# Kernel tuning notes

Measured on AMD Instinct MI355X. Metric: run time of the kernel, lower is better.

## Reference

```python
import jax, jax.numpy as jnp
import numpy as np

N = 16      # num_nodes
D = 128     # embedding_dim
H = 8       # num_heads
F = 512     # feedforward_dim
L = 4       # num_layers
IN = 64     # per-node input dim (joint_pos 32 + joint_vel 32)
B = 16384   # batch


def _ln(x, g, b):
    m = x.mean(-1, keepdims=True)
    v = ((x - m) ** 2).mean(-1, keepdims=True)
    return (x - m) * jax.lax.rsqrt(v + 1e-5) * g + b


def setup_inputs() -> dict:
    key = jax.random.key(0)
    ks = jax.random.split(key, 24)
    s = 0.02
    inp = {
        'joint_pos': jax.random.normal(ks[0], (B, 32), jnp.float32),
        'joint_vel': jax.random.normal(ks[1], (B, 32), jnp.float32),
        'adjacency': jax.random.randint(ks[2], (N, N), 0, 2).astype(jnp.int32),
        # per-node embedder (distinct Linear per node, stacked)
        'embed_W': jax.random.normal(ks[3], (N, IN, D), jnp.float32) * s,
        'embed_b': jnp.zeros((N, D), jnp.float32),
        'pos_emb': jax.random.normal(ks[4], (N, D), jnp.float32) * s,
        # per-layer attention params, stacked over layer dim
        'Wq': jax.random.normal(ks[5], (L, D, D), jnp.float32) * s,
        'bq': jnp.zeros((L, D), jnp.float32),
        'Wk': jax.random.normal(ks[6], (L, D, D), jnp.float32) * s,
        'bk': jnp.zeros((L, D), jnp.float32),
        'Wv': jax.random.normal(ks[7], (L, D, D), jnp.float32) * s,
        'bv': jnp.zeros((L, D), jnp.float32),
        'Wo': jax.random.normal(ks[8], (L, D, D), jnp.float32) * s,
        'bo': jnp.zeros((L, D), jnp.float32),
        'ln1_g': jnp.ones((L, D), jnp.float32),
        'ln1_b': jnp.zeros((L, D), jnp.float32),
        'ln2_g': jnp.ones((L, D), jnp.float32),
        'ln2_b': jnp.zeros((L, D), jnp.float32),
        'W1': jax.random.normal(ks[9], (L, D, F), jnp.float32) * s,
        'b1': jnp.zeros((L, F), jnp.float32),
        'W2': jax.random.normal(ks[10], (L, F, D), jnp.float32) * s,
        'b2': jnp.zeros((L, D), jnp.float32),
    }
    return inp


def reference(joint_pos, joint_vel, adjacency, embed_W, embed_b, pos_emb,
              Wq, bq, Wk, bk, Wv, bv, Wo, bo,
              ln1_g, ln1_b, ln2_g, ln2_b, W1, b1, W2, b2):
    # adjacency with forced self-loops -> additive attention mask [N, N]
    adj = adjacency.astype(bool) | jnp.eye(N, dtype=bool)
    mask = jnp.where(adj, 0.0, -jnp.inf).astype(jnp.float32)

    # every node sees the full concatenated obs (list-variant obs_node_dict)
    feats = jnp.concatenate([joint_pos, joint_vel], axis=-1)        # [B, IN]
    # distinct per-node linear embedders, batched as one einsum
    x = jnp.einsum('bi,nio->bno', feats, embed_W) + embed_b + pos_emb  # [B, N, D]

    dh = D // H
    scale = 1.0 / (dh ** 0.5)
    for l in range(L):  # BoT-Hard: mask on every layer; pre-LN
        h = _ln(x, ln1_g[l], ln1_b[l])
        q = (h @ Wq[l] + bq[l]).reshape(-1, N, H, dh)
        k = (h @ Wk[l] + bk[l]).reshape(-1, N, H, dh)
        v = (h @ Wv[l] + bv[l]).reshape(-1, N, H, dh)
        s = jnp.einsum('bnhd,bmhd->bhnm', q, k) * scale + mask       # [B, H, N, N]
        a = jax.nn.softmax(s, axis=-1)
        o = jnp.einsum('bhnm,bmhd->bnhd', a, v).reshape(-1, N, D)
        x = x + o @ Wo[l] + bo[l]
        h2 = _ln(x, ln2_g[l], ln2_b[l])
        x = x + jax.nn.relu(h2 @ W1[l] + b1[l]) @ W2[l] + b2[l]
    return x
```

## Files before the change

### kernel.cpp

```cpp
#include <hip/hip_runtime.h>
#include <stdint.h>

typedef __bf16 bf16;
typedef bf16 bf16x8 __attribute__((ext_vector_type(8)));
typedef bf16 bf16x4 __attribute__((ext_vector_type(4)));
typedef float f32x4 __attribute__((ext_vector_type(4)));
typedef uint32_t u32;
typedef uint8_t u8;

#define B_TOT 16384
#define SWG 8
#define NWGS (B_TOT / SWG)

__device__ __forceinline__ f32x4 mfma32(bf16x8 a, bf16x8 b, f32x4 c) {
  return __builtin_amdgcn_mfma_f32_16x16x32_bf16(a, b, c, 0, 0, 0);
}
__device__ __forceinline__ bf16x8 zero8() {
  bf16x8 v;
#pragma unroll
  for (int j = 0; j < 8; j++) v[j] = (bf16)0.f;
  return v;
}

__device__ __forceinline__ void bar_lg() {
  __builtin_amdgcn_sched_barrier(0);
  asm volatile("s_waitcnt lgkmcnt(0)" ::: "memory");
  __builtin_amdgcn_s_barrier();
  __builtin_amdgcn_sched_barrier(0);
}
__device__ __forceinline__ void bar_v0() {
  __builtin_amdgcn_sched_barrier(0);
  asm volatile("s_waitcnt vmcnt(0) lgkmcnt(0)" ::: "memory");
  __builtin_amdgcn_s_barrier();
  __builtin_amdgcn_sched_barrier(0);
}
__device__ __forceinline__ void bar_v2() {
  __builtin_amdgcn_sched_barrier(0);
  asm volatile("s_waitcnt vmcnt(2) lgkmcnt(0)" ::: "memory");
  __builtin_amdgcn_s_barrier();
  __builtin_amdgcn_sched_barrier(0);
}

__device__ __forceinline__ void stage16(const u8* __restrict__ src, int rowstride, int colbase,
                                        u8* dst, int tid) {
  __builtin_amdgcn_sched_barrier(0);
#pragma unroll
  for (int rr = 0; rr < 2; ++rr) {
    u32 o = (u32)(rr * 512 + tid) * 16u;
    u32 row = o >> 7, cb = o & 0x7Fu;
    const u8* s = src + (size_t)row * (size_t)rowstride + (size_t)colbase
                      + (size_t)(cb ^ ((row & 7u) << 4));
    __builtin_amdgcn_global_load_lds((const __attribute__((address_space(1))) u32*)s,
                                     (__attribute__((address_space(3))) u32*)(dst + o),
                                     16, 0, 0);
  }
}

__device__ __forceinline__ void st_row(u8* base, int row, int col, bf16 v) {
  *(bf16*)(base + (u32)(row * 256) + (u32)((2 * col) ^ ((row & 15) << 4))) = v;
}

__device__ __forceinline__ void loadA_rm(const u8* R, int g, int c, bf16x8 a[2][4]) {
  const u32 sw = (u32)c << 4;
#pragma unroll
  for (int mt = 0; mt < 2; ++mt)
#pragma unroll
    for (int ks = 0; ks < 4; ++ks)
      a[mt][ks] = *(const bf16x8*)(R + (u32)((mt * 16 + c) * 256)
                                     + (((u32)(ks * 64 + g * 16)) ^ sw));
}

__device__ __forceinline__ void gemm_half(const u8* Wb, int khalf, const bf16x8 a[2][4],
                                          f32x4 acc[2][4], int nh, int g, int c) {
  const u32 sw = (u32)(c & 7) << 4;
#pragma unroll
  for (int ksl = 0; ksl < 2; ++ksl) {
    int ks = khalf * 2 + ksl;
#pragma unroll
    for (int nt = 0; nt < 4; ++nt) {
      bf16x8 b = *(const bf16x8*)(Wb + (u32)((nh * 64 + nt * 16 + c) * 128)
                                     + (((u32)(ksl * 64 + g * 16)) ^ sw));
      acc[0][nt] = mfma32(a[0][ks], b, acc[0][nt]);
      acc[1][nt] = mfma32(a[1][ks], b, acc[1][nt]);
    }
  }
}

template <bool RELU>
__device__ __forceinline__ void epi_rm(const f32x4 acc[2][4], const float* __restrict__ bias,
                                       u8* Rdst, int nh, int g, int c) {
#pragma unroll
  for (int nt = 0; nt < 4; ++nt) {
    int col = nh * 64 + nt * 16 + c;
    float bb = bias[col];
#pragma unroll
    for (int mt = 0; mt < 2; ++mt)
#pragma unroll
      for (int r = 0; r < 4; ++r) {
        float v = acc[mt][nt][r] + bb;
        if (RELU) v = fmaxf(v, 0.f);
        st_row(Rdst, mt * 16 + 4 * g + r, col, (bf16)v);
      }
  }
}

__device__ __forceinline__ void pack4(const f32x4 v, u32& w0, u32& w1) {
  union { bf16 h[2]; u32 u; } t0, t1;
  t0.h[0] = (bf16)v[0]; t0.h[1] = (bf16)v[1];
  t1.h[0] = (bf16)v[2]; t1.h[1] = (bf16)v[3];
  w0 = t0.u; w1 = t1.u;
}

__device__ __forceinline__ bf16x8 Rfrag(u32 w0, u32 w1, int g, int c) {
  int s0 = 32 * g + c;
  int s1 = 32 * g + 16 + c;
  u32 a0 = (u32)__shfl((int)w0, s0);
  u32 a1 = (u32)__shfl((int)w1, s0);
  u32 a2 = (u32)__shfl((int)w0, s1);
  u32 a3 = (u32)__shfl((int)w1, s1);
  union { u32 u[4]; bf16x8 v; } r;
  bool ok = (g < 2);
  r.u[0] = ok ? a0 : 0u; r.u[1] = ok ? a1 : 0u;
  r.u[2] = ok ? a2 : 0u; r.u[3] = ok ? a3 : 0u;
  return r.v;
}

__device__ __forceinline__ void ln_part(const f32x4 x[2][4], float sS[2][4], float sS2[2][4]) {
#pragma unroll
  for (int mt = 0; mt < 2; ++mt) {
    f32x4 a = {0.f, 0.f, 0.f, 0.f}, b = {0.f, 0.f, 0.f, 0.f};
#pragma unroll
    for (int nt = 0; nt < 4; ++nt) { a += x[mt][nt]; b += x[mt][nt] * x[mt][nt]; }
#pragma unroll
    for (int r = 0; r < 4; ++r) {
      float s = a[r], s2 = b[r];
#pragma unroll
      for (int off = 1; off < 16; off <<= 1) { s += __shfl_xor(s, off); s2 += __shfl_xor(s2, off); }
      sS[mt][r] = s; sS2[mt][r] = s2;
    }
  }
}

__global__ void __launch_bounds__(512, 2)
bot_main(const int* __restrict__ adj,
         const float* __restrict__ embB, const float* __restrict__ posE,
         const float* __restrict__ pbq, const float* __restrict__ pbk,
         const float* __restrict__ pbv, const float* __restrict__ pbo,
         const float* __restrict__ l1g, const float* __restrict__ l1b,
         const float* __restrict__ l2g, const float* __restrict__ l2b,
         const float* __restrict__ pb1, const float* __restrict__ pb2,
         const bf16* __restrict__ feats, const bf16* __restrict__ embWT,
         const bf16* __restrict__ wqT, const bf16* __restrict__ wkT,
         const bf16* __restrict__ wvT, const bf16* __restrict__ woT,
         const bf16* __restrict__ w1T, const bf16* __restrict__ w2T,
         float* __restrict__ out) {
  __shared__ u8 smem[163840];
  const int tid = threadIdx.x;
  const int w = tid >> 6, lane = tid & 63, g = lane >> 4, c = lane & 15;
  const int p = w >> 1, nh = w & 1;
  const int S0 = blockIdx.x * SWG;

  u8* pairb = smem + p * 24576;
  u8* RA = pairb;
  u8* Rq = pairb + 8192;
  u8* Rk = pairb + 16384;
  u8* WB0 = smem + 98304;
  u8* WB1 = smem + 114688;
  u8* WB2 = smem + 131072;
  u8* WB3 = smem + 147456;
  float* scr = (float*)Rk;

  float maskT[4];
#pragma unroll
  for (int r = 0; r < 4; ++r) {
    int m = 4 * g + r;
    maskT[r] = (adj[c * 16 + m] != 0 || c == m) ? 0.f : -1e9f;
  }

  {
    float* x0 = (float*)smem;
    f32x4 ea[16] = {};
    bf16x8 af[2];
#pragma unroll
    for (int ks = 0; ks < 2; ++ks)
      af[ks] = *(const bf16x8*)(feats + (size_t)(S0 + (c & 7)) * 64 + ks * 32 + g * 8);
#pragma unroll
    for (int nt = 0; nt < 16; ++nt) {
#pragma unroll
      for (int ks = 0; ks < 2; ++ks) {
        bf16x8 bw = *(const bf16x8*)(embWT + (size_t)(w * 256 + nt * 16 + c) * 64 + ks * 32 + g * 8);
        ea[nt] = mfma32(af[ks], bw, ea[nt]);
      }
    }
    if (g < 2) {
#pragma unroll
      for (int nt = 0; nt < 16; ++nt)
#pragma unroll
        for (int r = 0; r < 4; ++r)
          x0[(4 * g + r) * 2048 + w * 256 + nt * 16 + c] = ea[nt][r];
    }
  }
  __syncthreads();

  f32x4 x[2][4];
  {
    const float* x0 = (const float*)smem;
#pragma unroll
    for (int nt = 0; nt < 4; ++nt)
#pragma unroll
      for (int r = 0; r < 4; ++r) {
        int n = 4 * g + r, d = nh * 64 + nt * 16 + c;
        float eb = embB[n * 128 + d] + posE[n * 128 + d];
#pragma unroll
        for (int mt = 0; mt < 2; ++mt)
          x[mt][nt][r] = x0[(2 * p + mt) * 2048 + n * 128 + d] + eb;
      }
  }
  __syncthreads();

  bf16x8 Ah[2][4], Ah2[2][4], Au[2][4];

#pragma unroll 1
  for (int l = 0; l < 4; ++l) {
    const u8* Wq_l = (const u8*)(wqT + (size_t)l * 16384);
    const u8* Wk_l = (const u8*)(wkT + (size_t)l * 16384);
    const u8* Wv_l = (const u8*)(wvT + (size_t)l * 16384);
    const u8* Wo_l = (const u8*)(woT + (size_t)l * 16384);
    const u8* W1_l = (const u8*)(w1T + (size_t)l * 65536);
    const u8* W2_l = (const u8*)(w2T + (size_t)l * 65536);

    float sS[2][4], sS2[2][4], mean[2][4], rstd[2][4];

    ln_part(x, sS, sS2);
    if (c == 0) {
#pragma unroll
      for (int mt = 0; mt < 2; ++mt)
#pragma unroll
        for (int r = 0; r < 4; ++r) {
          int row = mt * 16 + 4 * g + r;
          scr[(row * 2 + nh) * 2 + 0] = sS[mt][r];
          scr[(row * 2 + nh) * 2 + 1] = sS2[mt][r];
        }
    }
    stage16(Wq_l, 256, 0, WB0, tid);
    bar_lg();

#pragma unroll
    for (int mt = 0; mt < 2; ++mt)
#pragma unroll
      for (int r = 0; r < 4; ++r) {
        int row = mt * 16 + 4 * g + r;
        float s = sS[mt][r] + scr[(row * 2 + (1 - nh)) * 2 + 0];
        float s2 = sS2[mt][r] + scr[(row * 2 + (1 - nh)) * 2 + 1];
        float mu = s * (1.f / 128.f);
        float va = s2 * (1.f / 128.f) - mu * mu;
        mean[mt][r] = mu; rstd[mt][r] = rsqrtf(va + 1e-5f);
      }
#pragma unroll
    for (int nt = 0; nt < 4; ++nt) {
      int col = nh * 64 + nt * 16 + c;
      float gg = l1g[l * 128 + col], bb = l1b[l * 128 + col];
#pragma unroll
      for (int mt = 0; mt < 2; ++mt)
#pragma unroll
        for (int r = 0; r < 4; ++r)
          st_row(RA, mt * 16 + 4 * g + r, col,
                 (bf16)((x[mt][nt][r] - mean[mt][r]) * rstd[mt][r] * gg + bb));
    }
    stage16(Wq_l, 256, 128, WB1, tid);
    bar_v2();

    f32x4 acc[2][4];
    loadA_rm(RA, g, c, Ah);
#pragma unroll
    for (int mt = 0; mt < 2; ++mt)
#pragma unroll
      for (int nt = 0; nt < 4; ++nt) acc[mt][nt] = (f32x4){0.f, 0.f, 0.f, 0.f};
    gemm_half(WB0, 0, Ah, acc, nh, g, c);
    stage16(Wk_l, 256, 0, WB2, tid);
    bar_v2();

    gemm_half(WB1, 1, Ah, acc, nh, g, c);
    epi_rm<false>(acc, pbq + l * 128, Rq, nh, g, c);
    stage16(Wk_l, 256, 128, WB3, tid);
    bar_v2();

#pragma unroll
    for (int mt = 0; mt < 2; ++mt)
#pragma unroll
      for (int nt = 0; nt < 4; ++nt) acc[mt][nt] = (f32x4){0.f, 0.f, 0.f, 0.f};
    gemm_half(WB2, 0, Ah, acc, nh, g, c);
    stage16(Wv_l, 256, 0, WB0, tid);
    bar_v2();

    gemm_half(WB3, 1, Ah, acc, nh, g, c);
    epi_rm<false>(acc, pbk + l * 128, Rk, nh, g, c);
    stage16(Wv_l, 256, 128, WB1, tid);
    bar_v2();

#pragma unroll
    for (int mt = 0; mt < 2; ++mt)
#pragma unroll
      for (int nt = 0; nt < 4; ++nt) acc[mt][nt] = (f32x4){0.f, 0.f, 0.f, 0.f};
    gemm_half(WB0, 0, Ah, acc, nh, g, c);
    bar_v0();

    bf16x8 Vf[2][4];
    gemm_half(WB1, 1, Ah, acc, nh, g, c);
#pragma unroll
    for (int nt = 0; nt < 4; ++nt) {
      float bb = pbv[l * 128 + nh * 64 + nt * 16 + c];
#pragma unroll
      for (int mt = 0; mt < 2; ++mt) {
        f32x4 v;
#pragma unroll
        for (int r = 0; r < 4; ++r) v[r] = acc[mt][nt][r] + bb;
        u32 w0, w1; pack4(v, w0, w1);
        Vf[mt][nt] = Rfrag(w0, w1, g, c);
      }
    }
    stage16(Wo_l, 256, 0, WB2, tid);
    bar_lg();

    {
      const f32x4 zz = {0.f, 0.f, 0.f, 0.f};
      const u32 swa = (u32)c << 4;
#pragma unroll
      for (int hh = 0; hh < 4; ++hh) {
        const int gh = nh * 4 + hh;
        bf16x8 qf[2], kf[2];
#pragma unroll
        for (int mt = 0; mt < 2; ++mt) {
          if (g < 2) {
            qf[mt] = *(const bf16x8*)(Rq + (u32)((mt * 16 + c) * 256)
                                         + (((u32)(gh * 32 + g * 16)) ^ swa));
            kf[mt] = *(const bf16x8*)(Rk + (u32)((mt * 16 + c) * 256)
                                         + (((u32)(gh * 32 + g * 16)) ^ swa));
          } else { qf[mt] = zero8(); kf[mt] = zero8(); }
        }
#pragma unroll
        for (int mt = 0; mt < 2; ++mt) {
          f32x4 st = mfma32(kf[mt], qf[mt], zz);
          float pr[4];
#pragma unroll
          for (int r = 0; r < 4; ++r) pr[r] = st[r] * 0.25f + maskT[r];
          float mx = fmaxf(fmaxf(pr[0], pr[1]), fmaxf(pr[2], pr[3]));
          mx = fmaxf(mx, __shfl_xor(mx, 16));
          mx = fmaxf(mx, __shfl_xor(mx, 32));
          float sm = 0.f;
#pragma unroll
          for (int r = 0; r < 4; ++r) { pr[r] = __expf(pr[r] - mx); sm += pr[r]; }
          sm += __shfl_xor(sm, 16);
          sm += __shfl_xor(sm, 32);
          float pinv = __fdividef(1.f, sm);
          f32x4 pv;
#pragma unroll
          for (int r = 0; r < 4; ++r) pv[r] = pr[r] * pinv;
          u32 w0, w1; pack4(pv, w0, w1);
          bf16x8 Pf = Rfrag(w0, w1, g, c);
          f32x4 oo = mfma32(Vf[mt][hh], Pf, zz);
          pack4(oo, w0, w1);
          bf16x8 Of = Rfrag(w0, w1, g, c);
          if (g < 2)
            *(bf16x8*)(Rq + (u32)((mt * 16 + c) * 256)
                          + (((u32)(gh * 32 + g * 16)) ^ swa)) = Of;
        }
      }
    }
    stage16(Wo_l, 256, 128, WB3, tid);
    bar_v2();

    loadA_rm(Rq, g, c, Ah);
    gemm_half(WB2, 0, Ah, x, nh, g, c);
    bar_v0();

    gemm_half(WB3, 1, Ah, x, nh, g, c);
#pragma unroll
    for (int nt = 0; nt < 4; ++nt) {
      float bb = pbo[l * 128 + nh * 64 + nt * 16 + c];
#pragma unroll
      for (int mt = 0; mt < 2; ++mt)
#pragma unroll
        for (int r = 0; r < 4; ++r) x[mt][nt][r] += bb;
    }
    ln_part(x, sS, sS2);
    if (c == 0) {
#pragma unroll
      for (int mt = 0; mt < 2; ++mt)
#pragma unroll
        for (int r = 0; r < 4; ++r) {
          int row = mt * 16 + 4 * g + r;
          scr[(row * 2 + nh) * 2 + 0] = sS[mt][r];
          scr[(row * 2 + nh) * 2 + 1] = sS2[mt][r];
        }
    }
    stage16(W1_l, 256, 0, WB0, tid);
    bar_lg();

#pragma unroll
    for (int mt = 0; mt < 2; ++mt)
#pragma unroll
      for (int r = 0; r < 4; ++r) {
        int row = mt * 16 + 4 * g + r;
        float s = sS[mt][r] + scr[(row * 2 + (1 - nh)) * 2 + 0];
        float s2 = sS2[mt][r] + scr[(row * 2 + (1 - nh)) * 2 + 1];
        float mu = s * (1.f / 128.f);
        float va = s2 * (1.f / 128.f) - mu * mu;
        mean[mt][r] = mu; rstd[mt][r] = rsqrtf(va + 1e-5f);
      }
#pragma unroll
    for (int nt = 0; nt < 4; ++nt) {
      int col = nh * 64 + nt * 16 + c;
      float gg = l2g[l * 128 + col], bb = l2b[l * 128 + col];
#pragma unroll
      for (int mt = 0; mt < 2; ++mt)
#pragma unroll
        for (int r = 0; r < 4; ++r)
          st_row(RA, mt * 16 + 4 * g + r, col,
                 (bf16)((x[mt][nt][r] - mean[mt][r]) * rstd[mt][r] * gg + bb));
    }
    stage16(W1_l, 256, 128, WB1, tid);
    bar_v2();

#pragma unroll 1
    for (int fc = 0; fc < 4; ++fc) {
      f32x4 uacc[2][4];
#pragma unroll
      for (int mt = 0; mt < 2; ++mt)
#pragma unroll
        for (int nt = 0; nt < 4; ++nt) uacc[mt][nt] = (f32x4){0.f, 0.f, 0.f, 0.f};
      if (fc == 0) loadA_rm(RA, g, c, Ah2);
      gemm_half(WB0, 0, Ah2, uacc, nh, g, c);
      stage16(W2_l, 1024, fc * 256, WB2, tid);
      bar_v2();
      gemm_half(WB1, 1, Ah2, uacc, nh, g, c);
      epi_rm<true>(uacc, pb1 + l * 512 + fc * 128, Rq, nh, g, c);
      stage16(W2_l, 1024, fc * 256 + 128, WB3, tid);
      bar_v2();
      loadA_rm(Rq, g, c, Au);
      gemm_half(WB2, 0, Au, x, nh, g, c);
      if (fc < 3) { stage16(W1_l + (fc + 1) * 32768, 256, 0, WB0, tid); bar_v2(); }
      else bar_v0();
      gemm_half(WB3, 1, Au, x, nh, g, c);
      if (fc < 3) { stage16(W1_l + (fc + 1) * 32768, 256, 128, WB1, tid); bar_v2(); }
      else {
#pragma unroll
        for (int nt = 0; nt < 4; ++nt) {
          float bb = pb2[l * 128 + nh * 64 + nt * 16 + c];
#pragma unroll
          for (int mt = 0; mt < 2; ++mt)
#pragma unroll
            for (int r = 0; r < 4; ++r) x[mt][nt][r] += bb;
        }
        bar_lg();
      }
    }
  }

#pragma unroll
  for (int nt = 0; nt < 4; ++nt) {
    int col = nh * 64 + nt * 16 + c;
#pragma unroll
    for (int mt = 0; mt < 2; ++mt)
      *(f32x4*)(pairb + mt * 8192 + col * 64 + g * 16) = x[mt][nt];
  }
  bar_lg();
  {
    const int smp = S0 + 2 * p + nh;
    const u8* src = pairb + nh * 8192;
#pragma unroll
    for (int it = 0; it < 8; ++it) {
      int n = it * 2 + (lane >> 5);
      int slot = lane & 31;
      f32x4 v;
#pragma unroll
      for (int e = 0; e < 4; ++e)
        v[e] = *(const float*)(src + (u32)((slot * 4 + e) * 64 + n * 4));
      *(f32x4*)(out + (size_t)smp * 2048 + n * 128 + slot * 4) = v;
    }
  }
}

__global__ void prep_feats_k(const float* __restrict__ pos, const float* __restrict__ vel,
                             bf16* __restrict__ feats) {
  int i = blockIdx.x * 256 + threadIdx.x;
  if (i >= B_TOT * 64) return;
  int b = i >> 6, k = i & 63;
  float v = (k < 32) ? pos[b * 32 + k] : vel[b * 32 + (k - 32)];
  feats[i] = (bf16)v;
}

__global__ void prep_tr_k(const float* __restrict__ src, bf16* __restrict__ dst,
                          int R, int C, int total) {
  int i = blockIdx.x * 256 + threadIdx.x;
  if (i >= total) return;
  int rc = R * C;
  int m = i / rc, rem = i % rc;
  int cc = rem / R, rr = rem % R;
  dst[i] = (bf16)src[(size_t)m * rc + rr * C + cc];
}

extern "C" void kernel_launch(void* const* d_in, const int* in_sizes, int n_in,
                              void* d_out, int out_size, void* d_ws, size_t ws_size,
                              hipStream_t stream) {
  const float* jp  = (const float*)d_in[0];
  const float* jv  = (const float*)d_in[1];
  const int*   adj = (const int*)d_in[2];
  const float* eW  = (const float*)d_in[3];
  const float* eB  = (const float*)d_in[4];
  const float* pE  = (const float*)d_in[5];
  const float* Wq  = (const float*)d_in[6];  const float* bq = (const float*)d_in[7];
  const float* Wk  = (const float*)d_in[8];  const float* bk = (const float*)d_in[9];
  const float* Wv  = (const float*)d_in[10]; const float* bv = (const float*)d_in[11];
  const float* Wo  = (const float*)d_in[12]; const float* bo = (const float*)d_in[13];
  const float* g1  = (const float*)d_in[14]; const float* be1 = (const float*)d_in[15];
  const float* g2  = (const float*)d_in[16]; const float* be2 = (const float*)d_in[17];
  const float* W1  = (const float*)d_in[18]; const float* b1 = (const float*)d_in[19];
  const float* W2  = (const float*)d_in[20]; const float* b2 = (const float*)d_in[21];

  bf16* ws    = (bf16*)d_ws;
  bf16* feats = ws;
  bf16* embWT = ws + 1048576;
  bf16* wqT   = embWT + 131072;
  bf16* wkT   = wqT + 65536;
  bf16* wvT   = wkT + 65536;
  bf16* woT   = wvT + 65536;
  bf16* w1T   = woT + 65536;
  bf16* w2T   = w1T + 262144;

  prep_feats_k<<<(B_TOT * 64 + 255) / 256, 256, 0, stream>>>(jp, jv, feats);
  prep_tr_k<<<512, 256, 0, stream>>>(eW, embWT, 64, 128, 131072);
  prep_tr_k<<<256, 256, 0, stream>>>(Wq, wqT, 128, 128, 65536);
  prep_tr_k<<<256, 256, 0, stream>>>(Wk, wkT, 128, 128, 65536);
  prep_tr_k<<<256, 256, 0, stream>>>(Wv, wvT, 128, 128, 65536);
  prep_tr_k<<<256, 256, 0, stream>>>(Wo, woT, 128, 128, 65536);
  prep_tr_k<<<1024, 256, 0, stream>>>(W1, w1T, 128, 512, 262144);
  prep_tr_k<<<1024, 256, 0, stream>>>(W2, w2T, 512, 128, 262144);

  bot_main<<<NWGS, 512, 0, stream>>>(adj, eB, pE, bq, bk, bv, bo,
                                     g1, be1, g2, be2, b1, b2,
                                     feats, embWT, wqT, wkT, wvT, woT, w1T, w2T,
                                     (float*)d_out);
}
```

Before: 1.047 ms.

## Halve workgroup to 4 samples and 256 threads, triple-buffer weight staging in LDS

Each workgroup now handles 4 batch samples with 256 threads instead of 8 samples with 512, cutting LDS per block from 160KB to 80KB so more blocks can be resident per CU. Weight staging drops from four LDS buffers to three, rotated through the FFN loop, and each thread issues four async loads per stage with matching vmcnt(4) waits. The embedding phase is split into two passes per wave. The aim is higher occupancy and better latency hiding, at the cost of each staged weight tile being reused by half as many samples, which doubles global and L2 weight traffic.

```diff
diff --git a/kernel.cpp b/kernel.cpp
--- a/kernel.cpp
+++ b/kernel.cpp
@@ -9,7 +9,7 @@
 typedef uint8_t u8;
 
 #define B_TOT 16384
-#define SWG 8
+#define SWG 4
 #define NWGS (B_TOT / SWG)
 
 __device__ __forceinline__ f32x4 mfma32(bf16x8 a, bf16x8 b, f32x4 c) {
@@ -34,9 +34,9 @@
   __builtin_amdgcn_s_barrier();
   __builtin_amdgcn_sched_barrier(0);
 }
-__device__ __forceinline__ void bar_v2() {
-  __builtin_amdgcn_sched_barrier(0);
-  asm volatile("s_waitcnt vmcnt(2) lgkmcnt(0)" ::: "memory");
+__device__ __forceinline__ void bar_v4() {
+  __builtin_amdgcn_sched_barrier(0);
+  asm volatile("s_waitcnt vmcnt(4) lgkmcnt(0)" ::: "memory");
   __builtin_amdgcn_s_barrier();
   __builtin_amdgcn_sched_barrier(0);
 }
@@ -45,8 +45,8 @@
                                         u8* dst, int tid) {
   __builtin_amdgcn_sched_barrier(0);
 #pragma unroll
-  for (int rr = 0; rr < 2; ++rr) {
-    u32 o = (u32)(rr * 512 + tid) * 16u;
+  for (int rr = 0; rr < 4; ++rr) {
+    u32 o = (u32)(rr * 256 + tid) * 16u;
     u32 row = o >> 7, cb = o & 0x7Fu;
     const u8* s = src + (size_t)row * (size_t)rowstride + (size_t)colbase
                       + (size_t)(cb ^ ((row & 7u) << 4));
@@ -141,7 +141,7 @@
   }
 }
 
-__global__ void __launch_bounds__(512, 2)
+__global__ void __launch_bounds__(256, 2)
 bot_main(const int* __restrict__ adj,
          const float* __restrict__ embB, const float* __restrict__ posE,
          const float* __restrict__ pbq, const float* __restrict__ pbk,
@@ -154,21 +154,19 @@
          const bf16* __restrict__ wvT, const bf16* __restrict__ woT,
          const bf16* __restrict__ w1T, const bf16* __restrict__ w2T,
          float* __restrict__ out) {
-  __shared__ u8 smem[163840];
+  __shared__ u8 smem[81920];
   const int tid = threadIdx.x;
   const int w = tid >> 6, lane = tid & 63, g = lane >> 4, c = lane & 15;
   const int p = w >> 1, nh = w & 1;
   const int S0 = blockIdx.x * SWG;
 
-  u8* pairb = smem + p * 24576;
-  u8* RA = pairb;
-  u8* Rq = pairb + 8192;
-  u8* Rk = pairb + 16384;
-  u8* WB0 = smem + 98304;
-  u8* WB1 = smem + 114688;
-  u8* WB2 = smem + 131072;
-  u8* WB3 = smem + 147456;
-  float* scr = (float*)Rk;
+  u8* pairb = smem + p * 16384;
+  u8* Th = pairb;
+  u8* Tq = pairb + 8192;
+  u8* WB0 = smem + 32768;
+  u8* WB1 = smem + 49152;
+  u8* WB2 = smem + 65536;
+  float* scr = (float*)Tq;
 
   float maskT[4];
 #pragma unroll
@@ -179,25 +177,29 @@
 
   {
     float* x0 = (float*)smem;
-    f32x4 ea[16] = {};
     bf16x8 af[2];
 #pragma unroll
     for (int ks = 0; ks < 2; ++ks)
-      af[ks] = *(const bf16x8*)(feats + (size_t)(S0 + (c & 7)) * 64 + ks * 32 + g * 8);
-#pragma unroll
-    for (int nt = 0; nt < 16; ++nt) {
-#pragma unroll
-      for (int ks = 0; ks < 2; ++ks) {
-        bf16x8 bw = *(const bf16x8*)(embWT + (size_t)(w * 256 + nt * 16 + c) * 64 + ks * 32 + g * 8);
-        ea[nt] = mfma32(af[ks], bw, ea[nt]);
-      }
-    }
-    if (g < 2) {
-#pragma unroll
-      for (int nt = 0; nt < 16; ++nt)
-#pragma unroll
-        for (int r = 0; r < 4; ++r)
-          x0[(4 * g + r) * 2048 + w * 256 + nt * 16 + c] = ea[nt][r];
+      af[ks] = *(const bf16x8*)(feats + (size_t)(S0 + (c & 3)) * 64 + ks * 32 + g * 8);
+#pragma unroll
+    for (int pp = 0; pp < 2; ++pp) {
+      f32x4 ea[16] = {};
+#pragma unroll
+      for (int nt = 0; nt < 16; ++nt) {
+#pragma unroll
+        for (int ks = 0; ks < 2; ++ks) {
+          bf16x8 bw = *(const bf16x8*)(embWT
+              + (size_t)(w * 512 + pp * 256 + nt * 16 + c) * 64 + ks * 32 + g * 8);
+          ea[nt] = mfma32(af[ks], bw, ea[nt]);
+        }
+      }
+      if (g == 0) {
+#pragma unroll
+        for (int nt = 0; nt < 16; ++nt)
+#pragma unroll
+          for (int r = 0; r < 4; ++r)
+            x0[r * 2048 + w * 512 + pp * 256 + nt * 16 + c] = ea[nt][r];
+      }
     }
   }
   __syncthreads();
@@ -243,7 +245,7 @@
         }
     }
     stage16(Wq_l, 256, 0, WB0, tid);
-    bar_lg();
+    bar_v4();
 
 #pragma unroll
     for (int mt = 0; mt < 2; ++mt)
@@ -264,49 +266,49 @@
       for (int mt = 0; mt < 2; ++mt)
 #pragma unroll
         for (int r = 0; r < 4; ++r)
-          st_row(RA, mt * 16 + 4 * g + r, col,
+          st_row(Th, mt * 16 + 4 * g + r, col,
                  (bf16)((x[mt][nt][r] - mean[mt][r]) * rstd[mt][r] * gg + bb));
     }
     stage16(Wq_l, 256, 128, WB1, tid);
-    bar_v2();
+    bar_v4();
 
     f32x4 acc[2][4];
-    loadA_rm(RA, g, c, Ah);
+    loadA_rm(Th, g, c, Ah);
 #pragma unroll
     for (int mt = 0; mt < 2; ++mt)
 #pragma unroll
       for (int nt = 0; nt < 4; ++nt) acc[mt][nt] = (f32x4){0.f, 0.f, 0.f, 0.f};
     gemm_half(WB0, 0, Ah, acc, nh, g, c);
     stage16(Wk_l, 256, 0, WB2, tid);
-    bar_v2();
+    bar_v4();
 
     gemm_half(WB1, 1, Ah, acc, nh, g, c);
-    epi_rm<false>(acc, pbq + l * 128, Rq, nh, g, c);
-    stage16(Wk_l, 256, 128, WB3, tid);
-    bar_v2();
+    epi_rm<false>(acc, pbq + l * 128, Tq, nh, g, c);
+    stage16(Wk_l, 256, 128, WB0, tid);
+    bar_v4();
 
 #pragma unroll
     for (int mt = 0; mt < 2; ++mt)
 #pragma unroll
       for (int nt = 0; nt < 4; ++nt) acc[mt][nt] = (f32x4){0.f, 0.f, 0.f, 0.f};
     gemm_half(WB2, 0, Ah, acc, nh, g, c);
-    stage16(Wv_l, 256, 0, WB0, tid);
-    bar_v2();
-
-    gemm_half(WB3, 1, Ah, acc, nh, g, c);
-    epi_rm<false>(acc, pbk + l * 128, Rk, nh, g, c);
-    stage16(Wv_l, 256, 128, WB1, tid);
-    bar_v2();
+    stage16(Wv_l, 256, 0, WB1, tid);
+    bar_v4();
+
+    gemm_half(WB0, 1, Ah, acc, nh, g, c);
+    epi_rm<false>(acc, pbk + l * 128, Th, nh, g, c);
+    stage16(Wv_l, 256, 128, WB2, tid);
+    bar_v4();
 
 #pragma unroll
     for (int mt = 0; mt < 2; ++mt)
 #pragma unroll
       for (int nt = 0; nt < 4; ++nt) acc[mt][nt] = (f32x4){0.f, 0.f, 0.f, 0.f};
-    gemm_half(WB0, 0, Ah, acc, nh, g, c);
+    gemm_half(WB1, 0, Ah, acc, nh, g, c);
     bar_v0();
 
     bf16x8 Vf[2][4];
-    gemm_half(WB1, 1, Ah, acc, nh, g, c);
+    gemm_half(WB2, 1, Ah, acc, nh, g, c);
 #pragma unroll
     for (int nt = 0; nt < 4; ++nt) {
       float bb = pbv[l * 128 + nh * 64 + nt * 16 + c];
@@ -319,8 +321,8 @@
         Vf[mt][nt] = Rfrag(w0, w1, g, c);
       }
     }
-    stage16(Wo_l, 256, 0, WB2, tid);
-    bar_lg();
+    stage16(Wo_l, 256, 0, WB0, tid);
+    bar_v4();
 
     {
       const f32x4 zz = {0.f, 0.f, 0.f, 0.f};
@@ -332,9 +334,9 @@
 #pragma unroll
         for (int mt = 0; mt < 2; ++mt) {
           if (g < 2) {
-            qf[mt] = *(const bf16x8*)(Rq + (u32)((mt * 16 + c) * 256)
+            qf[mt] = *(const bf16x8*)(Tq + (u32)((mt * 16 + c) * 256)
                                          + (((u32)(gh * 32 + g * 16)) ^ swa));
-            kf[mt] = *(const bf16x8*)(Rk + (u32)((mt * 16 + c) * 256)
+            kf[mt] = *(const bf16x8*)(Th + (u32)((mt * 16 + c) * 256)
                                          + (((u32)(gh * 32 + g * 16)) ^ swa));
           } else { qf[mt] = zero8(); kf[mt] = zero8(); }
         }
@@ -362,19 +364,19 @@
           pack4(oo, w0, w1);
           bf16x8 Of = Rfrag(w0, w1, g, c);
           if (g < 2)
-            *(bf16x8*)(Rq + (u32)((mt * 16 + c) * 256)
+            *(bf16x8*)(Tq + (u32)((mt * 16 + c) * 256)
                           + (((u32)(gh * 32 + g * 16)) ^ swa)) = Of;
         }
       }
     }
-    stage16(Wo_l, 256, 128, WB3, tid);
-    bar_v2();
-
-    loadA_rm(Rq, g, c, Ah);
-    gemm_half(WB2, 0, Ah, x, nh, g, c);
+    stage16(Wo_l, 256, 128, WB1, tid);
+    bar_v4();
+
+    loadA_rm(Tq, g, c, Ah);
+    gemm_half(WB0, 0, Ah, x, nh, g, c);
     bar_v0();
 
-    gemm_half(WB3, 1, Ah, x, nh, g, c);
+    gemm_half(WB1, 1, Ah, x, nh, g, c);
 #pragma unroll
     for (int nt = 0; nt < 4; ++nt) {
       float bb = pbo[l * 128 + nh * 64 + nt * 16 + c];
@@ -394,8 +396,8 @@
           scr[(row * 2 + nh) * 2 + 1] = sS2[mt][r];
         }
     }
-    stage16(W1_l, 256, 0, WB0, tid);
-    bar_lg();
+    stage16(W1_l, 256, 0, WB2, tid);
+    bar_v4();
 
 #pragma unroll
     for (int mt = 0; mt < 2; ++mt)
@@ -416,12 +418,13 @@
       for (int mt = 0; mt < 2; ++mt)
 #pragma unroll
         for (int r = 0; r < 4; ++r)
-          st_row(RA, mt * 16 + 4 * g + r, col,
+          st_row(Th, mt * 16 + 4 * g + r, col,
                  (bf16)((x[mt][nt][r] - mean[mt][r]) * rstd[mt][r] * gg + bb));
     }
-    stage16(W1_l, 256, 128, WB1, tid);
-    bar_v2();
-
+    stage16(W1_l, 256, 128, WB0, tid);
+    bar_v4();
+
+    u8 *bA = WB2, *bB = WB0, *bC = WB1;
 #pragma unroll 1
     for (int fc = 0; fc < 4; ++fc) {
       f32x4 uacc[2][4];
@@ -429,20 +432,20 @@
       for (int mt = 0; mt < 2; ++mt)
 #pragma unroll
         for (int nt = 0; nt < 4; ++nt) uacc[mt][nt] = (f32x4){0.f, 0.f, 0.f, 0.f};
-      if (fc == 0) loadA_rm(RA, g, c, Ah2);
-      gemm_half(WB0, 0, Ah2, uacc, nh, g, c);
-      stage16(W2_l, 1024, fc * 256, WB2, tid);
-      bar_v2();
-      gemm_half(WB1, 1, Ah2, uacc, nh, g, c);
-      epi_rm<true>(uacc, pb1 + l * 512 + fc * 128, Rq, nh, g, c);
-      stage16(W2_l, 1024, fc * 256 + 128, WB3, tid);
-      bar_v2();
-      loadA_rm(Rq, g, c, Au);
-      gemm_half(WB2, 0, Au, x, nh, g, c);
-      if (fc < 3) { stage16(W1_l + (fc + 1) * 32768, 256, 0, WB0, tid); bar_v2(); }
+      if (fc == 0) loadA_rm(Th, g, c, Ah2);
+      gemm_half(bA, 0, Ah2, uacc, nh, g, c);
+      stage16(W2_l, 1024, fc * 256, bC, tid);
+      bar_v4();
+      gemm_half(bB, 1, Ah2, uacc, nh, g, c);
+      epi_rm<true>(uacc, pb1 + l * 512 + fc * 128, Tq, nh, g, c);
+      stage16(W2_l, 1024, fc * 256 + 128, bA, tid);
+      bar_v4();
+      loadA_rm(Tq, g, c, Au);
+      gemm_half(bC, 0, Au, x, nh, g, c);
+      if (fc < 3) { stage16(W1_l + (fc + 1) * 32768, 256, 0, bB, tid); bar_v4(); }
       else bar_v0();
-      gemm_half(WB3, 1, Au, x, nh, g, c);
-      if (fc < 3) { stage16(W1_l + (fc + 1) * 32768, 256, 128, WB1, tid); bar_v2(); }
+      gemm_half(bA, 1, Au, x, nh, g, c);
+      if (fc < 3) { stage16(W1_l + (fc + 1) * 32768, 256, 128, bC, tid); bar_v4(); }
       else {
 #pragma unroll
         for (int nt = 0; nt < 4; ++nt) {
@@ -454,6 +457,7 @@
         }
         bar_lg();
       }
+      u8* t = bA; bA = bB; bB = bC; bC = t;
     }
   }
 
@@ -537,7 +541,7 @@
   prep_tr_k<<<1024, 256, 0, stream>>>(W1, w1T, 128, 512, 262144);
   prep_tr_k<<<1024, 256, 0, stream>>>(W2, w2T, 512, 128, 262144);
 
-  bot_main<<<NWGS, 512, 0, stream>>>(adj, eB, pE, bq, bk, bv, bo,
+  bot_main<<<NWGS, 256, 0, stream>>>(adj, eB, pE, bq, bk, bv, bo,
                                      g1, be1, g2, be2, b1, b2,
                                      feats, embWT, wqT, wkT, wvT, woT, w1T, w2T,
                                      (float*)d_out);
```

Result: slower. 1.213 ms (+15.9%).

## Keep Q/K in registers, shrink LDS, and deepen weight prefetch pipeline

Applied to the files above, without the earlier changes.

Q and K projections are now computed transposed (weights as the A operand), and the results are packed straight into MFMA fragments via shuffles instead of being written to and re-read from LDS. This removes the Rk buffer and cuts shared memory from 160KB to 128KB. Weight staging is re-sequenced so Wo, W1 and W2 chunks are prefetched further ahead, with vmcnt(4) waits keeping two stages in flight. The final output stores use nontemporal hints. Register pressure rises from holding Qb and Ka fragments, and the deeper prefetch depends on the vmcnt accounting being exactly right.

```diff
diff --git a/kernel.cpp b/kernel.cpp
--- a/kernel.cpp
+++ b/kernel.cpp
@@ -15,12 +15,6 @@
 __device__ __forceinline__ f32x4 mfma32(bf16x8 a, bf16x8 b, f32x4 c) {
   return __builtin_amdgcn_mfma_f32_16x16x32_bf16(a, b, c, 0, 0, 0);
 }
-__device__ __forceinline__ bf16x8 zero8() {
-  bf16x8 v;
-#pragma unroll
-  for (int j = 0; j < 8; j++) v[j] = (bf16)0.f;
-  return v;
-}
 
 __device__ __forceinline__ void bar_lg() {
   __builtin_amdgcn_sched_barrier(0);
@@ -37,6 +31,12 @@
 __device__ __forceinline__ void bar_v2() {
   __builtin_amdgcn_sched_barrier(0);
   asm volatile("s_waitcnt vmcnt(2) lgkmcnt(0)" ::: "memory");
+  __builtin_amdgcn_s_barrier();
+  __builtin_amdgcn_sched_barrier(0);
+}
+__device__ __forceinline__ void bar_v4() {
+  __builtin_amdgcn_sched_barrier(0);
+  asm volatile("s_waitcnt vmcnt(4) lgkmcnt(0)" ::: "memory");
   __builtin_amdgcn_s_barrier();
   __builtin_amdgcn_sched_barrier(0);
 }
@@ -56,6 +56,10 @@
   }
 }
 
+__device__ __forceinline__ bf16x8 wread16(const u8* Wb, int row, u32 koff) {
+  return *(const bf16x8*)(Wb + (u32)(row * 128) + (koff ^ (((u32)row & 7u) << 4)));
+}
+
 __device__ __forceinline__ void st_row(u8* base, int row, int col, bf16 v) {
   *(bf16*)(base + (u32)(row * 256) + (u32)((2 * col) ^ ((row & 15) << 4))) = v;
 }
@@ -72,35 +76,15 @@
 
 __device__ __forceinline__ void gemm_half(const u8* Wb, int khalf, const bf16x8 a[2][4],
                                           f32x4 acc[2][4], int nh, int g, int c) {
-  const u32 sw = (u32)(c & 7) << 4;
 #pragma unroll
   for (int ksl = 0; ksl < 2; ++ksl) {
     int ks = khalf * 2 + ksl;
 #pragma unroll
     for (int nt = 0; nt < 4; ++nt) {
-      bf16x8 b = *(const bf16x8*)(Wb + (u32)((nh * 64 + nt * 16 + c) * 128)
-                                     + (((u32)(ksl * 64 + g * 16)) ^ sw));
+      bf16x8 b = wread16(Wb, nh * 64 + nt * 16 + c, (u32)(ksl * 64 + g * 16));
       acc[0][nt] = mfma32(a[0][ks], b, acc[0][nt]);
       acc[1][nt] = mfma32(a[1][ks], b, acc[1][nt]);
     }
-  }
-}
-
-template <bool RELU>
-__device__ __forceinline__ void epi_rm(const f32x4 acc[2][4], const float* __restrict__ bias,
-                                       u8* Rdst, int nh, int g, int c) {
-#pragma unroll
-  for (int nt = 0; nt < 4; ++nt) {
-    int col = nh * 64 + nt * 16 + c;
-    float bb = bias[col];
-#pragma unroll
-    for (int mt = 0; mt < 2; ++mt)
-#pragma unroll
-      for (int r = 0; r < 4; ++r) {
-        float v = acc[mt][nt][r] + bb;
-        if (RELU) v = fmaxf(v, 0.f);
-        st_row(Rdst, mt * 16 + 4 * g + r, col, (bf16)v);
-      }
   }
 }
 
@@ -154,21 +138,20 @@
          const bf16* __restrict__ wvT, const bf16* __restrict__ woT,
          const bf16* __restrict__ w1T, const bf16* __restrict__ w2T,
          float* __restrict__ out) {
-  __shared__ u8 smem[163840];
+  __shared__ u8 smem[131072];
   const int tid = threadIdx.x;
   const int w = tid >> 6, lane = tid & 63, g = lane >> 4, c = lane & 15;
   const int p = w >> 1, nh = w & 1;
   const int S0 = blockIdx.x * SWG;
 
-  u8* pairb = smem + p * 24576;
+  u8* pairb = smem + p * 16384;
   u8* RA = pairb;
   u8* Rq = pairb + 8192;
-  u8* Rk = pairb + 16384;
-  u8* WB0 = smem + 98304;
-  u8* WB1 = smem + 114688;
-  u8* WB2 = smem + 131072;
-  u8* WB3 = smem + 147456;
-  float* scr = (float*)Rk;
+  u8* WB0 = smem + 65536;
+  u8* WB1 = smem + 81920;
+  u8* WB2 = smem + 98304;
+  u8* WB3 = smem + 114688;
+  float* scr = (float*)Rq;
 
   float maskT[4];
 #pragma unroll
@@ -179,19 +162,18 @@
 
   {
     float* x0 = (float*)smem;
-    f32x4 ea[16] = {};
     bf16x8 af[2];
 #pragma unroll
     for (int ks = 0; ks < 2; ++ks)
       af[ks] = *(const bf16x8*)(feats + (size_t)(S0 + (c & 7)) * 64 + ks * 32 + g * 8);
-#pragma unroll
-    for (int nt = 0; nt < 16; ++nt) {
+    f32x4 ea[16] = {};
+#pragma unroll
+    for (int nt = 0; nt < 16; ++nt)
 #pragma unroll
       for (int ks = 0; ks < 2; ++ks) {
         bf16x8 bw = *(const bf16x8*)(embWT + (size_t)(w * 256 + nt * 16 + c) * 64 + ks * 32 + g * 8);
         ea[nt] = mfma32(af[ks], bw, ea[nt]);
       }
-    }
     if (g < 2) {
 #pragma unroll
       for (int nt = 0; nt < 16; ++nt)
@@ -230,6 +212,7 @@
     const u8* W2_l = (const u8*)(w2T + (size_t)l * 65536);
 
     float sS[2][4], sS2[2][4], mean[2][4], rstd[2][4];
+    const f32x4 zz = {0.f, 0.f, 0.f, 0.f};
 
     ln_part(x, sS, sS2);
     if (c == 0) {
@@ -270,42 +253,94 @@
     stage16(Wq_l, 256, 128, WB1, tid);
     bar_v2();
 
+    bf16x8 Qb[4][2], Ka[4][2], Vf[2][4];
+    {
+      f32x4 qacc[4][2];
+      loadA_rm(RA, g, c, Ah);
+#pragma unroll
+      for (int hh = 0; hh < 4; ++hh) {
+        int gh = nh * 4 + hh;
+#pragma unroll
+        for (int mt = 0; mt < 2; ++mt) qacc[hh][mt] = zz;
+#pragma unroll
+        for (int ksl = 0; ksl < 2; ++ksl) {
+          bf16x8 wf = wread16(WB0, gh * 16 + c, (u32)(ksl * 64 + g * 16));
+          qacc[hh][0] = mfma32(wf, Ah[0][ksl], qacc[hh][0]);
+          qacc[hh][1] = mfma32(wf, Ah[1][ksl], qacc[hh][1]);
+        }
+      }
+      stage16(Wk_l, 256, 0, WB2, tid);
+      bar_v2();
+
+#pragma unroll
+      for (int hh = 0; hh < 4; ++hh) {
+        int gh = nh * 4 + hh;
+#pragma unroll
+        for (int ksl = 0; ksl < 2; ++ksl) {
+          bf16x8 wf = wread16(WB1, gh * 16 + c, (u32)(ksl * 64 + g * 16));
+          qacc[hh][0] = mfma32(wf, Ah[0][2 + ksl], qacc[hh][0]);
+          qacc[hh][1] = mfma32(wf, Ah[1][2 + ksl], qacc[hh][1]);
+        }
+        const float* bql = pbq + l * 128 + gh * 16 + 4 * g;
+#pragma unroll
+        for (int mt = 0; mt < 2; ++mt) {
+          f32x4 v;
+#pragma unroll
+          for (int r = 0; r < 4; ++r) v[r] = qacc[hh][mt][r] + bql[r];
+          u32 w0, w1; pack4(v, w0, w1);
+          Qb[hh][mt] = Rfrag(w0, w1, g, c);
+        }
+      }
+      stage16(Wk_l, 256, 128, WB3, tid);
+      bar_v2();
+
+#pragma unroll
+      for (int hh = 0; hh < 4; ++hh) {
+        int gh = nh * 4 + hh;
+#pragma unroll
+        for (int mt = 0; mt < 2; ++mt) qacc[hh][mt] = zz;
+#pragma unroll
+        for (int ksl = 0; ksl < 2; ++ksl) {
+          bf16x8 wf = wread16(WB2, gh * 16 + c, (u32)(ksl * 64 + g * 16));
+          qacc[hh][0] = mfma32(wf, Ah[0][ksl], qacc[hh][0]);
+          qacc[hh][1] = mfma32(wf, Ah[1][ksl], qacc[hh][1]);
+        }
+      }
+      stage16(Wv_l, 256, 0, WB0, tid);
+      bar_v2();
+
+#pragma unroll
+      for (int hh = 0; hh < 4; ++hh) {
+        int gh = nh * 4 + hh;
+#pragma unroll
+        for (int ksl = 0; ksl < 2; ++ksl) {
+          bf16x8 wf = wread16(WB3, gh * 16 + c, (u32)(ksl * 64 + g * 16));
+          qacc[hh][0] = mfma32(wf, Ah[0][2 + ksl], qacc[hh][0]);
+          qacc[hh][1] = mfma32(wf, Ah[1][2 + ksl], qacc[hh][1]);
+        }
+        const float* bkl = pbk + l * 128 + gh * 16 + 4 * g;
+#pragma unroll
+        for (int mt = 0; mt < 2; ++mt) {
+          f32x4 v;
+#pragma unroll
+          for (int r = 0; r < 4; ++r) v[r] = qacc[hh][mt][r] + bkl[r];
+          u32 w0, w1; pack4(v, w0, w1);
+          Ka[hh][mt] = Rfrag(w0, w1, g, c);
+        }
+      }
+      stage16(Wv_l, 256, 128, WB1, tid);
+      bar_v2();
+    }
+
     f32x4 acc[2][4];
-    loadA_rm(RA, g, c, Ah);
 #pragma unroll
     for (int mt = 0; mt < 2; ++mt)
 #pragma unroll
-      for (int nt = 0; nt < 4; ++nt) acc[mt][nt] = (f32x4){0.f, 0.f, 0.f, 0.f};
+      for (int nt = 0; nt < 4; ++nt) acc[mt][nt] = zz;
     gemm_half(WB0, 0, Ah, acc, nh, g, c);
-    stage16(Wk_l, 256, 0, WB2, tid);
+    stage16(Wo_l, 256, 0, WB2, tid);
     bar_v2();
 
-    gemm_half(WB1, 1, Ah, acc, nh, g, c);
-    epi_rm<false>(acc, pbq + l * 128, Rq, nh, g, c);
-    stage16(Wk_l, 256, 128, WB3, tid);
-    bar_v2();
-
-#pragma unroll
-    for (int mt = 0; mt < 2; ++mt)
-#pragma unroll
-      for (int nt = 0; nt < 4; ++nt) acc[mt][nt] = (f32x4){0.f, 0.f, 0.f, 0.f};
-    gemm_half(WB2, 0, Ah, acc, nh, g, c);
-    stage16(Wv_l, 256, 0, WB0, tid);
-    bar_v2();
-
-    gemm_half(WB3, 1, Ah, acc, nh, g, c);
-    epi_rm<false>(acc, pbk + l * 128, Rk, nh, g, c);
-    stage16(Wv_l, 256, 128, WB1, tid);
-    bar_v2();
-
-#pragma unroll
-    for (int mt = 0; mt < 2; ++mt)
-#pragma unroll
-      for (int nt = 0; nt < 4; ++nt) acc[mt][nt] = (f32x4){0.f, 0.f, 0.f, 0.f};
-    gemm_half(WB0, 0, Ah, acc, nh, g, c);
-    bar_v0();
-
-    bf16x8 Vf[2][4];
     gemm_half(WB1, 1, Ah, acc, nh, g, c);
 #pragma unroll
     for (int nt = 0; nt < 4; ++nt) {
@@ -319,28 +354,14 @@
         Vf[mt][nt] = Rfrag(w0, w1, g, c);
       }
     }
-    stage16(Wo_l, 256, 0, WB2, tid);
-    bar_lg();
-
     {
-      const f32x4 zz = {0.f, 0.f, 0.f, 0.f};
       const u32 swa = (u32)c << 4;
 #pragma unroll
       for (int hh = 0; hh < 4; ++hh) {
         const int gh = nh * 4 + hh;
-        bf16x8 qf[2], kf[2];
 #pragma unroll
         for (int mt = 0; mt < 2; ++mt) {
-          if (g < 2) {
-            qf[mt] = *(const bf16x8*)(Rq + (u32)((mt * 16 + c) * 256)
-                                         + (((u32)(gh * 32 + g * 16)) ^ swa));
-            kf[mt] = *(const bf16x8*)(Rk + (u32)((mt * 16 + c) * 256)
-                                         + (((u32)(gh * 32 + g * 16)) ^ swa));
-          } else { qf[mt] = zero8(); kf[mt] = zero8(); }
-        }
-#pragma unroll
-        for (int mt = 0; mt < 2; ++mt) {
-          f32x4 st = mfma32(kf[mt], qf[mt], zz);
+          f32x4 st = mfma32(Ka[hh][mt], Qb[hh][mt], zz);
           float pr[4];
 #pragma unroll
           for (int r = 0; r < 4; ++r) pr[r] = st[r] * 0.25f + maskT[r];
@@ -372,7 +393,8 @@
 
     loadA_rm(Rq, g, c, Ah);
     gemm_half(WB2, 0, Ah, x, nh, g, c);
-    bar_v0();
+    stage16(W1_l, 256, 0, WB0, tid);
+    bar_v2();
 
     gemm_half(WB3, 1, Ah, x, nh, g, c);
 #pragma unroll
@@ -394,7 +416,7 @@
           scr[(row * 2 + nh) * 2 + 1] = sS2[mt][r];
         }
     }
-    stage16(W1_l, 256, 0, WB0, tid);
+    stage16(W1_l, 256, 128, WB1, tid);
     bar_lg();
 
 #pragma unroll
@@ -419,8 +441,8 @@
           st_row(RA, mt * 16 + 4 * g + r, col,
                  (bf16)((x[mt][nt][r] - mean[mt][r]) * rstd[mt][r] * gg + bb));
     }
-    stage16(W1_l, 256, 128, WB1, tid);
-    bar_v2();
+    stage16(W2_l, 1024, 0, WB2, tid);
+    bar_v4();
 
 #pragma unroll 1
     for (int fc = 0; fc < 4; ++fc) {
@@ -428,21 +450,30 @@
 #pragma unroll
       for (int mt = 0; mt < 2; ++mt)
 #pragma unroll
-        for (int nt = 0; nt < 4; ++nt) uacc[mt][nt] = (f32x4){0.f, 0.f, 0.f, 0.f};
+        for (int nt = 0; nt < 4; ++nt) uacc[mt][nt] = zz;
       if (fc == 0) loadA_rm(RA, g, c, Ah2);
       gemm_half(WB0, 0, Ah2, uacc, nh, g, c);
-      stage16(W2_l, 1024, fc * 256, WB2, tid);
-      bar_v2();
+      stage16(W2_l, 1024, fc * 256 + 128, WB3, tid);
+      bar_v4();
       gemm_half(WB1, 1, Ah2, uacc, nh, g, c);
-      epi_rm<true>(uacc, pb1 + l * 512 + fc * 128, Rq, nh, g, c);
-      stage16(W2_l, 1024, fc * 256 + 128, WB3, tid);
-      bar_v2();
+#pragma unroll
+      for (int nt = 0; nt < 4; ++nt) {
+        int col = nh * 64 + nt * 16 + c;
+        float bb = pb1[l * 512 + fc * 128 + col];
+#pragma unroll
+        for (int mt = 0; mt < 2; ++mt)
+#pragma unroll
+          for (int r = 0; r < 4; ++r)
+            st_row(Rq, mt * 16 + 4 * g + r, col, (bf16)fmaxf(uacc[mt][nt][r] + bb, 0.f));
+      }
+      if (fc < 3) { stage16(W1_l + (fc + 1) * 32768, 256, 0, WB0, tid); bar_v4(); }
+      else bar_v2();
       loadA_rm(Rq, g, c, Au);
       gemm_half(WB2, 0, Au, x, nh, g, c);
-      if (fc < 3) { stage16(W1_l + (fc + 1) * 32768, 256, 0, WB0, tid); bar_v2(); }
+      if (fc < 3) { stage16(W1_l + (fc + 1) * 32768, 256, 128, WB1, tid); bar_v4(); }
       else bar_v0();
       gemm_half(WB3, 1, Au, x, nh, g, c);
-      if (fc < 3) { stage16(W1_l + (fc + 1) * 32768, 256, 128, WB1, tid); bar_v2(); }
+      if (fc < 3) { stage16(W2_l, 1024, (fc + 1) * 256, WB2, tid); bar_v4(); }
       else {
 #pragma unroll
         for (int nt = 0; nt < 4; ++nt) {
@@ -476,7 +507,7 @@
 #pragma unroll
       for (int e = 0; e < 4; ++e)
         v[e] = *(const float*)(src + (u32)((slot * 4 + e) * 64 + n * 4));
-      *(f32x4*)(out + (size_t)smp * 2048 + n * 128 + slot * 4) = v;
+      __builtin_nontemporal_store(v, (f32x4*)(out + (size_t)smp * 2048 + n * 128 + slot * 4));
     }
   }
 }
```

Measured after the change: 1.374 ms. 31.3% more time.
